# Performance work log

Measured on AMD Instinct MI355X. Metric: run time of the kernel, lower is better.

The kernel has to match this reference:

```python
import jax, jax.numpy as jnp
import numpy as np

B, T, C, NH, RD = 128, 512, 384, 6, 16
HD = C // NH
SEQ_LEN = 512


def setup_inputs() -> dict:
    key = jax.random.key(0)
    kx, kqkv, kout = jax.random.split(key, 3)
    x = jax.random.normal(kx, (B, T, C), dtype=jnp.float32)
    # torch nn.Linear weights are [out_features, in_features]
    Wqkv = jax.random.normal(kqkv, (3 * C, C), dtype=jnp.float32) * 0.02
    Wout = jax.random.normal(kout, (C, C), dtype=jnp.float32) * 0.02
    freqs = 1.0 / (10000.0 ** (jnp.arange(0, RD, 2, dtype=jnp.float32) / RD))  # [RD//2]
    f = jnp.outer(jnp.arange(SEQ_LEN, dtype=jnp.float32), freqs)  # [SEQ_LEN, RD//2]
    cos = jnp.cos(f)[None, None]  # [1,1,SEQ_LEN,RD//2]
    sin = jnp.sin(f)[None, None]
    return {"x": x, "Wqkv": Wqkv, "Wout": Wout, "cos": cos, "sin": sin}


def _rope(t, c, s, rd):
    # t: [B, NH, T, HD]; partial rotary on first rd channels
    r, p = t[..., :rd], t[..., rd:]
    r1, r2 = r[..., : rd // 2], r[..., rd // 2:]
    rot = jnp.concatenate([r1 * c - r2 * s, r2 * c + r1 * s], axis=-1)
    return jnp.concatenate([rot, p], axis=-1)


def reference(x, Wqkv, Wout, cos, sin):
    b, t, c = x.shape
    nh, hd, rd = NH, c // NH, RD
    qkv = jnp.einsum("btc,dc->btd", x, Wqkv).reshape(b, t, 3, nh, hd)
    q, k, v = (jnp.transpose(qkv[:, :, i], (0, 2, 1, 3)) for i in range(3))  # [b,nh,t,hd]
    cc = cos[:, :, :t]
    ss = sin[:, :, :t]
    q = _rope(q, cc, ss, rd)
    k = _rope(k, cc, ss, rd)
    scale = 1.0 / jnp.sqrt(jnp.asarray(hd, dtype=x.dtype))
    scores = jnp.einsum("bhqd,bhkd->bhqk", q, k) * scale
    causal = jnp.tril(jnp.ones((t, t), dtype=bool))
    scores = jnp.where(causal, scores, jnp.finfo(scores.dtype).min)
    att = jax.nn.softmax(scores, axis=-1)
    o = jnp.einsum("bhqk,bhkd->bhqd", att, v)  # [b,nh,t,hd]
    o = jnp.transpose(o, (0, 2, 1, 3)).reshape(b, t, c)
    return jnp.einsum("btc,dc->btd", o, Wout)
```

## Files before the change

### kernel.cpp

```cpp
#include <hip/hip_runtime.h>

#define B_DIM 128
#define T_DIM 512
#define C_DIM 384
#define NH_DIM 6
#define HD_DIM 64
#define QKV_LD 1152

typedef __bf16 bf16x8 __attribute__((ext_vector_type(8)));
typedef __bf16 bf16x4 __attribute__((ext_vector_type(4)));
typedef float f32x4 __attribute__((ext_vector_type(4)));

#define K_SCALE 0.18033688011112042f

__device__ __forceinline__ void gload_lds16(const __bf16* g, __bf16* l) {
  __builtin_amdgcn_global_load_lds(
      (const __attribute__((address_space(1))) void*)g,
      (__attribute__((address_space(3))) void*)l, 16, 0, 0);
}

#define X_F4 6291456
#define WQKV_F4 110592
#define WOUT_F4 36864
__global__ __launch_bounds__(256) void cast_all(const float* __restrict__ x,
                                                const float* __restrict__ wqkv,
                                                const float* __restrict__ wout,
                                                __bf16* __restrict__ xb,
                                                __bf16* __restrict__ wqkvb,
                                                __bf16* __restrict__ woutb) {
  int i = blockIdx.x * blockDim.x + threadIdx.x;
  const float4* src;
  bf16x4* dst;
  if (i < X_F4) {
    src = (const float4*)x + i;
    dst = (bf16x4*)xb + i;
  } else if (i < X_F4 + WQKV_F4) {
    src = (const float4*)wqkv + (i - X_F4);
    dst = (bf16x4*)wqkvb + (i - X_F4);
  } else {
    src = (const float4*)wout + (i - X_F4 - WQKV_F4);
    dst = (bf16x4*)woutb + (i - X_F4 - WOUT_F4 - (WQKV_F4 - WOUT_F4));
  }
  float4 v = *src;
  bf16x4 o;
  o[0] = (__bf16)v.x; o[1] = (__bf16)v.y; o[2] = (__bf16)v.z; o[3] = (__bf16)v.w;
  *dst = o;
}

__global__ __launch_bounds__(256) void gemm_bt(const __bf16* __restrict__ A,
                                               const __bf16* __restrict__ Bm,
                                               __bf16* __restrict__ Cb,
                                               float* __restrict__ Cf,
                                               const float* __restrict__ cosp,
                                               const float* __restrict__ sinp,
                                               int M, int N, int K) {
  __shared__ __attribute__((aligned(16))) __bf16 As[128 * 32];
  __shared__ __attribute__((aligned(16))) __bf16 Bs[128 * 32];
  const int m0 = blockIdx.y * 128;
  const int n0 = blockIdx.x * 128;
  const int tid = threadIdx.x;
  const int wave = tid >> 6;
  const int lane = tid & 63;
  const int lr = lane & 15;
  const int quad = lane >> 4;
  const int wm = (wave & 1) * 64;
  const int wn = (wave >> 1) * 64;
  const int ca0 = wave * 2, ca1 = wave * 2 + 1;
  const int srow = lane >> 2;
  const int row0 = ca0 * 16 + srow, row1 = ca1 * 16 + srow;
  const int slot = (lane & 3) ^ ((lane >> 3) & 3);
  const int rs = (quad ^ ((lr >> 1) & 3)) * 8;
  f32x4 acc[4][4] = {};
  for (int k0 = 0; k0 < K; k0 += 32) {
    __syncthreads();
    gload_lds16(&A[(size_t)(m0 + row0) * K + k0 + slot * 8], &As[ca0 * 512]);
    gload_lds16(&A[(size_t)(m0 + row1) * K + k0 + slot * 8], &As[ca1 * 512]);
    gload_lds16(&Bm[(size_t)(n0 + row0) * K + k0 + slot * 8], &Bs[ca0 * 512]);
    gload_lds16(&Bm[(size_t)(n0 + row1) * K + k0 + slot * 8], &Bs[ca1 * 512]);
    __syncthreads();
    bf16x8 af[4], bf[4];
#pragma unroll
    for (int i = 0; i < 4; ++i)
      af[i] = *(bf16x8*)&As[(wm + i * 16 + lr) * 32 + rs];
#pragma unroll
    for (int j = 0; j < 4; ++j)
      bf[j] = *(bf16x8*)&Bs[(wn + j * 16 + lr) * 32 + rs];
#pragma unroll
    for (int i = 0; i < 4; ++i)
#pragma unroll
      for (int j = 0; j < 4; ++j)
        acc[i][j] = __builtin_amdgcn_mfma_f32_16x16x32_bf16(af[i], bf[j], acc[i][j], 0, 0, 0);
  }
  const bool doRope = (cosp != nullptr);
#pragma unroll
  for (int i = 0; i < 4; ++i) {
#pragma unroll
    for (int j = 0; j < 4; ++j) {
      int gm = m0 + wm + i * 16 + quad * 4;
      int gn = n0 + wn + j * 16 + lr;
      if (Cf) {
#pragma unroll
        for (int r = 0; r < 4; ++r) Cf[(size_t)(gm + r) * N + gn] = acc[i][j][r];
      } else {
        const int cbase = n0 + wn + j * 16;
        const bool ropeBlk = doRope && (cbase < 2 * C_DIM) && ((cbase & 63) == 0);
        const float qs = (doRope && cbase < C_DIM) ? K_SCALE : 1.0f;
        if (ropeBlk) {
#pragma unroll
          for (int r = 0; r < 4; ++r) {
            float v = acc[i][j][r];
            float p = __shfl_xor(v, 8, 64);
            int t = (gm + r) & (T_DIM - 1);
            float c = cosp[t * 8 + (lr & 7)];
            float s = sinp[t * 8 + (lr & 7)];
            v = (lr & 8) ? __builtin_fmaf(v, c, p * s)
                         : __builtin_fmaf(v, c, -p * s);
            Cb[(size_t)(gm + r) * N + gn] = (__bf16)(v * qs);
          }
        } else {
#pragma unroll
          for (int r = 0; r < 4; ++r)
            Cb[(size_t)(gm + r) * N + gn] = (__bf16)(acc[i][j][r] * qs);
        }
      }
    }
  }
}

__global__ __launch_bounds__(256) void transpose_v(const __bf16* __restrict__ qkv,
                                                   __bf16* __restrict__ vt) {
  __shared__ __attribute__((aligned(16))) __bf16 Tl[64][72];
  const int tt = blockIdx.x;
  const int h = blockIdx.y;
  const int b = blockIdx.z;
  const int tid = threadIdx.x;
  const __bf16* src = qkv + (size_t)b * T_DIM * QKV_LD + 2 * C_DIM + h * HD_DIM;
#pragma unroll
  for (int i = 0; i < 2; ++i) {
    int c = tid + i * 256;
    int row = c >> 3, cc = (c & 7) * 8;
    *(bf16x8*)&Tl[row][cc] = *(const bf16x8*)&src[(size_t)(tt * 64 + row) * QKV_LD + cc];
  }
  __syncthreads();
  __bf16* dst = vt + (size_t)(b * NH_DIM + h) * HD_DIM * T_DIM + tt * 64;
#pragma unroll
  for (int i = 0; i < 2; ++i) {
    int c = tid + i * 256;
    int drow = c >> 3, tc = (c & 7) * 8;
    bf16x8 v;
#pragma unroll
    for (int j = 0; j < 8; ++j) v[j] = Tl[tc + j][drow];
    *(bf16x8*)&dst[(size_t)drow * T_DIM + tc] = v;
  }
}

__global__ __launch_bounds__(256) void attn_kernel(const __bf16* __restrict__ qkv,
                                                   const __bf16* __restrict__ vt,
                                                   __bf16* __restrict__ o) {
  __shared__ __attribute__((aligned(16))) __bf16 K0s[64 * 64];
  __shared__ __attribute__((aligned(16))) __bf16 K1s[64 * 64];
  __shared__ __attribute__((aligned(16))) __bf16 V0s[64 * 64];
  __shared__ __attribute__((aligned(16))) __bf16 V1s[64 * 64];
  const int pair = blockIdx.x;
  const int qlo = pair, qhi = 7 - pair;
  const int h = blockIdx.y;
  const int b = blockIdx.z;
  const int tid = threadIdx.x;
  const int wave = tid >> 6;
  const int lane = tid & 63;
  const int lr = lane & 15;
  const int quad = lane >> 4;
  const __bf16* qbase = qkv + (size_t)b * T_DIM * QKV_LD + h * HD_DIM;
  const __bf16* kbase = qbase + C_DIM;
  const __bf16* vtb = vt + (size_t)(b * NH_DIM + h) * HD_DIM * T_DIM;
  const int qrow_lo = qlo * 64 + wave * 16;
  const int qrow_hi = qhi * 64 + wave * 16;
  bf16x8 qfl[2], qfh[2];
#pragma unroll
  for (int ks = 0; ks < 2; ++ks) {
    qfl[ks] = *(const bf16x8*)&qbase[(size_t)(qrow_lo + lr) * QKV_LD + ks * 32 + quad * 8];
    qfh[ks] = *(const bf16x8*)&qbase[(size_t)(qrow_hi + lr) * QKV_LD + ks * 32 + quad * 8];
  }
  f32x4 oaL[4] = {}, oaH[4] = {};
  f32x4 lL = {}, lH = {};
  bf16x8 vones;
#pragma unroll
  for (int e = 0; e < 8; ++e) vones[e] = (__bf16)1.0f;
  const int skey = (((lane >> 3) & 3) << 1) | (wave & 1);
  const int gsl = ((lane & 7) ^ skey) * 8;
  const int grA = wave * 8 + (lane >> 3);
  const int grB = grA + 32;
  const int ldsA = wave * 512;
  const int ldsB = (wave + 4) * 512;
  auto stage = [&](int kt, __bf16* KT, __bf16* VT) {
    const __bf16* ks = kbase + (size_t)(kt * 64) * QKV_LD;
    const __bf16* vs = vtb + kt * 64;
    gload_lds16(&ks[(size_t)grA * QKV_LD + gsl], KT + ldsA);
    gload_lds16(&ks[(size_t)grB * QKV_LD + gsl], KT + ldsB);
    gload_lds16(&vs[(size_t)grA * T_DIM + gsl], VT + ldsA);
    gload_lds16(&vs[(size_t)grB * T_DIM + gsl], VT + ldsB);
  };
  const int keyK = ((lr & 3) << 1) | ((lr >> 2) & 1);
  const int keyV = ((lr & 3) << 1) | ((lr >> 3) & 1);
  const int swK0 = (quad ^ keyK) * 8, swK1 = ((4 + quad) ^ keyK) * 8;
  const int swV0 = (quad ^ keyV) * 8, swV1 = ((4 + quad) ^ keyV) * 8;
  const int rkbase = ((lr >> 2) & 3) * 8 + (lr & 3);
  auto body = [&](const __bf16* KT, const __bf16* VT, const bf16x8 (&qf)[2],
                  f32x4 (&oa)[4], f32x4& lacc, int myq, bool diag, int kt) {
    f32x4 sj[4];
#pragma unroll
    for (int j = 0; j < 4; ++j) {
      const int rK = (j >> 1) * 32 + (j & 1) * 4 + rkbase;
      bf16x8 kf0 = *(const bf16x8*)&KT[rK * 64 + swK0];
      bf16x8 kf1 = *(const bf16x8*)&KT[rK * 64 + swK1];
      f32x4 z = {};
      z = __builtin_amdgcn_mfma_f32_16x16x32_bf16(kf0, qf[0], z, 0, 0, 0);
      z = __builtin_amdgcn_mfma_f32_16x16x32_bf16(kf1, qf[1], z, 0, 0, 0);
      sj[j] = z;
    }
    if (diag) {
#pragma unroll
      for (int j = 0; j < 4; ++j)
#pragma unroll
        for (int r = 0; r < 4; ++r) {
          int key = kt * 64 + (j >> 1) * 32 + quad * 8 + (j & 1) * 4 + r;
          if (key > myq) sj[j][r] = -3.0e38f;
        }
    }
    bf16x8 pf0, pf1;
#pragma unroll
    for (int j = 0; j < 4; ++j)
#pragma unroll
      for (int r = 0; r < 4; ++r) {
        float pv = exp2f(sj[j][r]);
        const int jj = (j & 1) * 4 + r;
        if (j < 2) pf0[jj] = (__bf16)pv; else pf1[jj] = (__bf16)pv;
      }
#pragma unroll
    for (int dt = 0; dt < 4; ++dt) {
      bf16x8 vf0 = *(const bf16x8*)&VT[(dt * 16 + lr) * 64 + swV0];
      bf16x8 vf1 = *(const bf16x8*)&VT[(dt * 16 + lr) * 64 + swV1];
      oa[dt] = __builtin_amdgcn_mfma_f32_16x16x32_bf16(pf0, vf0, oa[dt], 0, 0, 0);
      oa[dt] = __builtin_amdgcn_mfma_f32_16x16x32_bf16(pf1, vf1, oa[dt], 0, 0, 0);
    }
    lacc = __builtin_amdgcn_mfma_f32_16x16x32_bf16(pf0, vones, lacc, 0, 0, 0);
    lacc = __builtin_amdgcn_mfma_f32_16x16x32_bf16(pf1, vones, lacc, 0, 0, 0);
  };
  stage(0, K0s, V0s);
  __syncthreads();
  int kt = 0;
  while (true) {
    if (kt < qhi) stage(kt + 1, K1s, V1s);
    if (kt <= qlo) body(K0s, V0s, qfl, oaL, lL, qrow_lo + lr, kt == qlo, kt);
    body(K0s, V0s, qfh, oaH, lH, qrow_hi + lr, kt == qhi, kt);
    __syncthreads();
    ++kt;
    if (kt > qhi) break;
    if (kt < qhi) stage(kt + 1, K0s, V0s);
    if (kt <= qlo) body(K1s, V1s, qfl, oaL, lL, qrow_lo + lr, kt == qlo, kt);
    body(K1s, V1s, qfh, oaH, lH, qrow_hi + lr, kt == qhi, kt);
    __syncthreads();
    ++kt;
    if (kt > qhi) break;
  }
#pragma unroll
  for (int r = 0; r < 4; ++r) {
    float ilL = 1.0f / lL[r];
    float ilH = 1.0f / lH[r];
#pragma unroll
    for (int dt = 0; dt < 4; ++dt) {
      size_t rowL = (size_t)b * T_DIM + qrow_lo + quad * 4 + r;
      size_t rowH = (size_t)b * T_DIM + qrow_hi + quad * 4 + r;
      o[rowL * C_DIM + h * HD_DIM + dt * 16 + lr] = (__bf16)(oaL[dt][r] * ilL);
      o[rowH * C_DIM + h * HD_DIM + dt * 16 + lr] = (__bf16)(oaH[dt][r] * ilH);
    }
  }
}

extern "C" void kernel_launch(void* const* d_in, const int* in_sizes, int n_in,
                              void* d_out, int out_size, void* d_ws, size_t ws_size,
                              hipStream_t stream) {
  const float* x    = (const float*)d_in[0];
  const float* wqkv = (const float*)d_in[1];
  const float* wout = (const float*)d_in[2];
  const float* cosp = (const float*)d_in[3];
  const float* sinp = (const float*)d_in[4];
  float* out = (float*)d_out;

  char* ws = (char*)d_ws;
  __bf16* xb    = (__bf16*)(ws);
  __bf16* wqkvb = (__bf16*)(ws + 50331648);
  __bf16* woutb = (__bf16*)(ws + 51216384);
  __bf16* qkvb  = (__bf16*)(ws + 51511296);
  __bf16* ob    = (__bf16*)(ws + 202506240);
  __bf16* vtb   = xb;

  const int M = B_DIM * T_DIM;

  cast_all<<<25152, 256, 0, stream>>>(x, wqkv, wout, xb, wqkvb, woutb);

  gemm_bt<<<dim3(QKV_LD / 128, M / 128), 256, 0, stream>>>(
      xb, wqkvb, qkvb, (float*)nullptr, cosp, sinp, M, QKV_LD, C_DIM);

  transpose_v<<<dim3(T_DIM / 64, NH_DIM, B_DIM), 256, 0, stream>>>(qkvb, vtb);

  attn_kernel<<<dim3(4, NH_DIM, B_DIM), 256, 0, stream>>>(qkvb, vtb, ob);

  gemm_bt<<<dim3(C_DIM / 128, M / 128), 256, 0, stream>>>(
      ob, woutb, (__bf16*)nullptr, out, (const float*)nullptr, (const float*)nullptr,
      M, C_DIM, C_DIM);
}
```

Measured before the change: 412.5 us.

## Fuse x fp32-to-bf16 cast into QKV GEMM and swizzle block order for XCDs

Removes the separate cast of the large x activation by having the QKV GEMM load fp32 A directly into registers, convert to bf16 and store into LDS, with a register prefetch of the next k-tile. The cast kernel now only converts weights. Both the GEMM and the attention kernel remap block IDs with a stride-8 swizzle so that neighbouring tiles land on the same XCD, aiming for better L2 reuse. The A path no longer uses direct global-to-LDS loads, which adds VGPR pressure and conversion ALU work.

```diff
diff --git a/kernel.cpp b/kernel.cpp
--- a/kernel.cpp
+++ b/kernel.cpp
@@ -19,27 +19,21 @@
       (__attribute__((address_space(3))) void*)l, 16, 0, 0);
 }
 
-#define X_F4 6291456
 #define WQKV_F4 110592
 #define WOUT_F4 36864
-__global__ __launch_bounds__(256) void cast_all(const float* __restrict__ x,
-                                                const float* __restrict__ wqkv,
-                                                const float* __restrict__ wout,
-                                                __bf16* __restrict__ xb,
-                                                __bf16* __restrict__ wqkvb,
-                                                __bf16* __restrict__ woutb) {
+__global__ __launch_bounds__(256) void cast_w(const float* __restrict__ wqkv,
+                                              const float* __restrict__ wout,
+                                              __bf16* __restrict__ wqkvb,
+                                              __bf16* __restrict__ woutb) {
   int i = blockIdx.x * blockDim.x + threadIdx.x;
   const float4* src;
   bf16x4* dst;
-  if (i < X_F4) {
-    src = (const float4*)x + i;
-    dst = (bf16x4*)xb + i;
-  } else if (i < X_F4 + WQKV_F4) {
-    src = (const float4*)wqkv + (i - X_F4);
-    dst = (bf16x4*)wqkvb + (i - X_F4);
+  if (i < WQKV_F4) {
+    src = (const float4*)wqkv + i;
+    dst = (bf16x4*)wqkvb + i;
   } else {
-    src = (const float4*)wout + (i - X_F4 - WQKV_F4);
-    dst = (bf16x4*)woutb + (i - X_F4 - WOUT_F4 - (WQKV_F4 - WOUT_F4));
+    src = (const float4*)wout + (i - WQKV_F4);
+    dst = (bf16x4*)woutb + (i - WQKV_F4);
   }
   float4 v = *src;
   bf16x4 o;
@@ -48,6 +42,7 @@
 }
 
 __global__ __launch_bounds__(256) void gemm_bt(const __bf16* __restrict__ A,
+                                               const float* __restrict__ Af,
                                                const __bf16* __restrict__ Bm,
                                                __bf16* __restrict__ Cb,
                                                float* __restrict__ Cf,
@@ -56,8 +51,12 @@
                                                int M, int N, int K) {
   __shared__ __attribute__((aligned(16))) __bf16 As[128 * 32];
   __shared__ __attribute__((aligned(16))) __bf16 Bs[128 * 32];
-  const int m0 = blockIdx.y * 128;
-  const int n0 = blockIdx.x * 128;
+  const int nwg = gridDim.x * gridDim.y;
+  const int bid = blockIdx.x + gridDim.x * blockIdx.y;
+  const int per = nwg >> 3;
+  const int swz = (bid & 7) * per + (bid >> 3);
+  const int m0 = (swz / gridDim.x) * 128;
+  const int n0 = (swz % gridDim.x) * 128;
   const int tid = threadIdx.x;
   const int wave = tid >> 6;
   const int lane = tid & 63;
@@ -70,14 +69,38 @@
   const int row0 = ca0 * 16 + srow, row1 = ca1 * 16 + srow;
   const int slot = (lane & 3) ^ ((lane >> 3) & 3);
   const int rs = (quad ^ ((lr >> 1) & 3)) * 8;
+  float4 ar[2][2];
+  auto loadA = [&](int k0) {
+#pragma unroll
+    for (int c = 0; c < 2; ++c) {
+      const int row = (wave * 2 + c) * 16 + srow;
+      const float4* p = (const float4*)&Af[(size_t)(m0 + row) * K + k0 + slot * 8];
+      ar[c][0] = p[0];
+      ar[c][1] = p[1];
+    }
+  };
+  if (Af) loadA(0);
   f32x4 acc[4][4] = {};
   for (int k0 = 0; k0 < K; k0 += 32) {
     __syncthreads();
-    gload_lds16(&A[(size_t)(m0 + row0) * K + k0 + slot * 8], &As[ca0 * 512]);
-    gload_lds16(&A[(size_t)(m0 + row1) * K + k0 + slot * 8], &As[ca1 * 512]);
+    if (Af) {
+#pragma unroll
+      for (int c = 0; c < 2; ++c) {
+        bf16x8 w;
+        w[0] = (__bf16)ar[c][0].x; w[1] = (__bf16)ar[c][0].y;
+        w[2] = (__bf16)ar[c][0].z; w[3] = (__bf16)ar[c][0].w;
+        w[4] = (__bf16)ar[c][1].x; w[5] = (__bf16)ar[c][1].y;
+        w[6] = (__bf16)ar[c][1].z; w[7] = (__bf16)ar[c][1].w;
+        *(bf16x8*)&As[(wave * 2 + c) * 512 + lane * 8] = w;
+      }
+    } else {
+      gload_lds16(&A[(size_t)(m0 + row0) * K + k0 + slot * 8], &As[ca0 * 512]);
+      gload_lds16(&A[(size_t)(m0 + row1) * K + k0 + slot * 8], &As[ca1 * 512]);
+    }
     gload_lds16(&Bm[(size_t)(n0 + row0) * K + k0 + slot * 8], &Bs[ca0 * 512]);
     gload_lds16(&Bm[(size_t)(n0 + row1) * K + k0 + slot * 8], &Bs[ca1 * 512]);
     __syncthreads();
+    if (Af && k0 + 32 < K) loadA(k0 + 32);
     bf16x8 af[4], bf[4];
 #pragma unroll
     for (int i = 0; i < 4; ++i)
@@ -161,10 +184,12 @@
   __shared__ __attribute__((aligned(16))) __bf16 K1s[64 * 64];
   __shared__ __attribute__((aligned(16))) __bf16 V0s[64 * 64];
   __shared__ __attribute__((aligned(16))) __bf16 V1s[64 * 64];
-  const int pair = blockIdx.x;
+  const int bid = blockIdx.x;
+  const int swz = (bid & 7) * 384 + (bid >> 3);
+  const int pair = swz & 3;
+  const int h = (swz >> 2) % NH_DIM;
+  const int b = swz / (4 * NH_DIM);
   const int qlo = pair, qhi = 7 - pair;
-  const int h = blockIdx.y;
-  const int b = blockIdx.z;
   const int tid = threadIdx.x;
   const int wave = tid >> 6;
   const int lane = tid & 63;
@@ -288,25 +313,25 @@
   float* out = (float*)d_out;
 
   char* ws = (char*)d_ws;
-  __bf16* xb    = (__bf16*)(ws);
+  __bf16* vtb   = (__bf16*)(ws);
   __bf16* wqkvb = (__bf16*)(ws + 50331648);
   __bf16* woutb = (__bf16*)(ws + 51216384);
   __bf16* qkvb  = (__bf16*)(ws + 51511296);
   __bf16* ob    = (__bf16*)(ws + 202506240);
-  __bf16* vtb   = xb;
 
   const int M = B_DIM * T_DIM;
 
-  cast_all<<<25152, 256, 0, stream>>>(x, wqkv, wout, xb, wqkvb, woutb);
+  cast_w<<<576, 256, 0, stream>>>(wqkv, wout, wqkvb, woutb);
 
   gemm_bt<<<dim3(QKV_LD / 128, M / 128), 256, 0, stream>>>(
-      xb, wqkvb, qkvb, (float*)nullptr, cosp, sinp, M, QKV_LD, C_DIM);
+      (const __bf16*)nullptr, x, wqkvb, qkvb, (float*)nullptr, cosp, sinp,
+      M, QKV_LD, C_DIM);
 
   transpose_v<<<dim3(T_DIM / 64, NH_DIM, B_DIM), 256, 0, stream>>>(qkvb, vtb);
 
-  attn_kernel<<<dim3(4, NH_DIM, B_DIM), 256, 0, stream>>>(qkvb, vtb, ob);
+  attn_kernel<<<3072, 256, 0, stream>>>(qkvb, vtb, ob);
 
   gemm_bt<<<dim3(C_DIM / 128, M / 128), 256, 0, stream>>>(
-      ob, woutb, (__bf16*)nullptr, out, (const float*)nullptr, (const float*)nullptr,
-      M, C_DIM, C_DIM);
-}
+      ob, (const float*)nullptr, woutb, (__bf16*)nullptr, out,
+      (const float*)nullptr, (const float*)nullptr, M, C_DIM, C_DIM);
+}
```

Result: no change. 415.2 us (+0.6%).
